# Kernel optimization log

Hardware: AMD Instinct MI355X
Metric: run time of the kernel (lower is better)

Reference implementation:

```python
import jax, jax.numpy as jnp
import numpy as np
import math

B, S, D, H = 4, 2048, 1024, 16

def setup_inputs() -> dict:
    key = jax.random.key(0)
    ks = jax.random.split(key, 8)
    scale = 1.0 / math.sqrt(D)
    return {
        "queries": jax.random.normal(ks[0], (B, S, D), dtype=jnp.float32),
        "keys": jax.random.normal(ks[1], (B, S, D), dtype=jnp.float32),
        "values": jax.random.normal(ks[2], (B, S, D), dtype=jnp.float32),
        "valid_len": jax.random.randint(ks[3], (B,), 1, S + 1, dtype=jnp.int32),
        "Wq": jax.random.normal(ks[4], (D, D), dtype=jnp.float32) * scale,
        "Wk": jax.random.normal(ks[5], (D, D), dtype=jnp.float32) * scale,
        "Wv": jax.random.normal(ks[6], (D, D), dtype=jnp.float32) * scale,
        "Wo": jax.random.normal(ks[7], (D, D), dtype=jnp.float32) * scale,
    }

def reference(queries, keys, values, valid_len, Wq, Wk, Wv, Wo):
    b, sq, _ = queries.shape
    sk = keys.shape[1]
    hd = D // H
    # projections + split heads -> [B, H, S, hd]
    q = (queries @ Wq).reshape(b, sq, H, hd).transpose(0, 2, 1, 3)
    k = (keys @ Wk).reshape(b, sk, H, hd).transpose(0, 2, 1, 3)
    v = (values @ Wv).reshape(b, sk, H, hd).transpose(0, 2, 1, 3)
    scores = jnp.einsum('bhqd,bhkd->bhqk', q, k) / math.sqrt(hd)
    # Source's sequence_mask uses query-dim length as maxlen: masks whole
    # query rows where q_pos >= valid_len (value -100000), then softmax over keys.
    row_ok = (jnp.arange(sq)[None, :] < valid_len[:, None])  # [B, Sq]
    scores = jnp.where(row_ok[:, None, :, None], scores, -100000.0)
    weights = jax.nn.softmax(scores, axis=-1)  # dropout=0.0 (eval)
    out = jnp.einsum('bhqk,bhkd->bhqd', weights, v)
    out = out.transpose(0, 2, 1, 3).reshape(b, sq, H * hd)
    return out @ Wo
```

## Files before the change

kernel.cpp:

```cpp
#include <hip/hip_runtime.h>
#include <hip/hip_bf16.h>

#define NB 4
#define NS 2048
#define ND 1024
#define NH 16
#define HDIM 64
#define NM (NB * NS)
#define MN_FULL ((size_t)NM * ND)

typedef short short8 __attribute__((ext_vector_type(8)));
typedef float f32x4 __attribute__((ext_vector_type(4)));
typedef float f32x16 __attribute__((ext_vector_type(16)));
typedef unsigned uint4v __attribute__((ext_vector_type(4)));

__device__ __forceinline__ short bf16rne(float f) {
    unsigned u = __builtin_bit_cast(unsigned, f);
    u += 0x7fff + ((u >> 16) & 1);
    return (short)(u >> 16);
}
__device__ __forceinline__ float bf2f(short s) {
    unsigned u = ((unsigned)(unsigned short)s) << 16;
    return __builtin_bit_cast(float, u);
}
__device__ __forceinline__ void gl_lds16(const short* g, short* l) {
    __builtin_amdgcn_global_load_lds(
        (const __attribute__((address_space(1))) void*)g,
        (__attribute__((address_space(3))) void*)l, 16, 0, 0);
}
__device__ __forceinline__ float fexp2(float x) {
#if __has_builtin(__builtin_amdgcn_exp2f)
    return __builtin_amdgcn_exp2f(x);
#else
    return exp2f(x);
#endif
}
__device__ __forceinline__ unsigned cvtpk(float a, float b) {
    unsigned d;
    asm("v_cvt_pk_bf16_f32 %0, %1, %2" : "=v"(d) : "v"(a), "v"(b));
    return d;
}
__device__ __forceinline__ void plswap(unsigned& x, unsigned& y) {
    asm("v_permlane32_swap_b32 %0, %1" : "+v"(x), "+v"(y));
}
__device__ __forceinline__ short8 mk8(unsigned a, unsigned b, unsigned c, unsigned d) {
    uint4v u = {a, b, c, d};
    return __builtin_bit_cast(short8, u);
}

__global__ __launch_bounds__(256)
void convA3(const float* __restrict__ A0, const float* __restrict__ A1,
            const float* __restrict__ A2, short* __restrict__ D0,
            short* __restrict__ D1, short* __restrict__ D2)
{
    const int z = blockIdx.z;
    const float* A = (z == 0) ? A0 : (z == 1) ? A1 : A2;
    short* D = (z == 0) ? D0 : (z == 1) ? D1 : D2;

    const size_t idx = (size_t)blockIdx.x * 256 + threadIdx.x;
    const int m = (int)(idx >> 7);
    const int k = (int)((idx & 127) << 3);
    const float* src = A + ((size_t)m << 10) + k;
    float4 x0 = *(const float4*)src;
    float4 x1 = *(const float4*)(src + 4);
    float xv[8] = {x0.x, x0.y, x0.z, x0.w, x1.x, x1.y, x1.z, x1.w};
    short8 hv;
#pragma unroll
    for (int j = 0; j < 8; ++j) hv[j] = bf16rne(xv[j]);
    const int ksw = (k & ~63) | ((k & 63) ^ ((m & 7) << 3));
    *(short8*)(D + ((size_t)m << 10) + ksw) = hv;
}

__global__ __launch_bounds__(256)
void convW4(const float* __restrict__ W0, const float* __restrict__ W1,
            const float* __restrict__ W2, const float* __restrict__ W3,
            short* __restrict__ Wb)
{
    const int z = blockIdx.z;
    const float* W = (z == 0) ? W0 : (z == 1) ? W1 : (z == 2) ? W2 : W3;
    short* Wh = Wb + (size_t)z * ND * ND;

    const int idx = blockIdx.x * 256 + threadIdx.x;
    const int n = idx & 1023;
    const int k = (idx >> 10) << 3;
    short8 hv;
#pragma unroll
    for (int j = 0; j < 8; ++j) hv[j] = bf16rne(W[(size_t)(k + j) * ND + n]);
    const int ksw = (k & ~63) | ((k & 63) ^ ((n & 7) << 3));
    *(short8*)(Wh + ((size_t)n << 10) + ksw) = hv;
}

template <int EPI>
__global__ __launch_bounds__(256, 3)
void gemm1(const short* __restrict__ Ah, const short* __restrict__ Bh,
           short* __restrict__ D1, float* __restrict__ Cf, float scale)
{
    __shared__ short lds[16384];
    short* AhS = lds;
    short* BhS = lds + 8192;

    const int t = threadIdx.x, w = t >> 6, l = t & 63;
    const int g = l >> 4, li = l & 15;
    const int wr = w >> 1, wc = w & 1;
    const size_t bm = (size_t)blockIdx.x * 128, bn = (size_t)blockIdx.y * 128;

    f32x4 acc[4][4];
#pragma unroll
    for (int i = 0; i < 4; ++i)
#pragma unroll
        for (int j = 0; j < 4; ++j) acc[i][j] = (f32x4){0.f, 0.f, 0.f, 0.f};

    const int srow = w * 32 + (l >> 3);
    const int schk = (l & 7) << 3;
    const short* pAh = Ah + (bm + srow) * 1024 + schk;
    const short* pBh = Bh + (bn + srow) * 1024 + schk;
    const int lbase = w * 32 * 64;

    for (int kt = 0; kt < 16; ++kt) {
        const int k0 = kt * 64;
        __syncthreads();
#pragma unroll
        for (int r = 0; r < 4; ++r) {
            const int go = r * 8 * 1024 + k0;
            const int lo_ = lbase + r * 512;
            gl_lds16(pAh + go, AhS + lo_);
            gl_lds16(pBh + go, BhS + lo_);
        }
        __syncthreads();
#pragma unroll
        for (int ks = 0; ks < 2; ++ks) {
            short8 fah[4], fbh[4];
#pragma unroll
            for (int i = 0; i < 4; ++i) {
                const int m = wr * 64 + i * 16 + li;
                const int c = (ks * 32 + g * 8) ^ ((m & 7) << 3);
                fah[i] = *(const short8*)&AhS[m * 64 + c];
                const int n = wc * 64 + i * 16 + li;
                const int cn = (ks * 32 + g * 8) ^ ((n & 7) << 3);
                fbh[i] = *(const short8*)&BhS[n * 64 + cn];
            }
#pragma unroll
            for (int i = 0; i < 4; ++i)
#pragma unroll
                for (int j = 0; j < 4; ++j)
                    acc[i][j] = __builtin_amdgcn_mfma_f32_16x16x32_bf16(fah[i], fbh[j], acc[i][j], 0, 0, 0);
        }
    }

    __syncthreads();
    float* Ofs = (float*)lds + w * 2048;
#pragma unroll
    for (int half = 0; half < 2; ++half) {
#pragma unroll
        for (int i = 0; i < 4; ++i)
#pragma unroll
            for (int jj = 0; jj < 2; ++jj)
#pragma unroll
                for (int r = 0; r < 4; ++r)
                    Ofs[(i * 16 + g * 4 + r) * 32 + jj * 16 + li] = acc[i][half * 2 + jj][r];
        if (EPI == 3) {
#pragma unroll
            for (int rr = 0; rr < 2; ++rr) {
                const int row = rr * 32 + (l >> 1);
                const int coff = (l & 1) * 16;
                const float* src = &Ofs[row * 32 + coff];
                short8 h0, h1;
#pragma unroll
                for (int jj = 0; jj < 8; ++jj) {
                    h0[jj] = bf16rne(src[jj] * scale);
                    h1[jj] = bf16rne(src[8 + jj] * scale);
                }
                const size_t rg = bm + wr * 64 + row;
                const size_t cg = bn + wc * 64 + half * 32 + coff;
                *(short8*)(D1 + rg * 1024 + cg)     = h0;
                *(short8*)(D1 + rg * 1024 + cg + 8) = h1;
            }
        } else if (EPI == 0) {
#pragma unroll
            for (int rr = 0; rr < 2; ++rr) {
                const int row = rr * 32 + (l >> 1);
                const int coff = (l & 1) * 16;
                const float* src = &Ofs[row * 32 + coff];
                const size_t rg = bm + wr * 64 + row;
                const size_t cg = bn + wc * 64 + half * 32 + coff;
#pragma unroll
                for (int q = 0; q < 4; ++q)
                    *(float4*)(Cf + rg * 1024 + cg + q * 4) = *(const float4*)(src + q * 4);
            }
        } else {
#pragma unroll
            for (int p = 0; p < 4; ++p) {
                const int nl = p * 16 + (l >> 2);
                const int mc = (l & 3) * 8;
                const float* src = &Ofs[nl * 32 + mc];
                short8 v;
#pragma unroll
                for (int jj = 0; jj < 8; ++jj) v[jj] = bf16rne(src[jj]);
                const int ng = (int)bm + wr * 64 + nl;
                const size_t mg = bn + wc * 64 + half * 32 + mc;
                const int h_ = ng >> 6, d_ = ng & 63;
                const int b_ = (int)(mg >> 11), s_ = (int)(mg & 2047);
                *(short8*)(D1 + (((size_t)(b_ * NH + h_) * HDIM + d_) << 11) + s_) = v;
            }
        }
    }
}

__global__ __launch_bounds__(256, 4)
void attn_mfma11(const short* __restrict__ Qh_g, const short* __restrict__ Kh_g,
                 const short* __restrict__ VT_g, const int* __restrict__ vlen_p,
                 short* __restrict__ AOh)
{
    __shared__ short smem[16384];
    short* Kb = smem;
    short* Vb = smem + 8192;

    const int t = threadIdx.x, w = t >> 6, l = t & 63;
    const int lh = l >> 5, lq = l & 31;

    const int lin = blockIdx.x;
    const int pair = (lin & 7) * 8 + (lin >> 7);
    const int qt = (lin >> 3) & 15;
    const int hd = pair & 15, b = pair >> 4;
    const int q0 = qt * 128;
    const int vlen = vlen_p[b];

    const short* Vbh = VT_g + (size_t)((b * NH + hd) * HDIM) * NS;

    if (q0 >= vlen) {
        float* fs = (float*)smem;
        const int d = t & 63, pc = t >> 6;
        const short* vrow = Vbh + (size_t)d * NS + pc * 512;
        float s = 0.f;
#pragma unroll 8
        for (int c = 0; c < 64; ++c) {
            short8 v = *(const short8*)(vrow + c * 8);
            float ps = 0.f;
#pragma unroll
            for (int j = 0; j < 8; ++j) ps += bf2f(v[j]);
            s += ps;
        }
        fs[pc * 64 + d] = s;
        __syncthreads();
        float* mv = fs + 256;
        if (t < 64)
            mv[t] = (fs[t] + fs[64 + t] + fs[128 + t] + fs[192 + t]) * (1.0f / 2048.0f);
        __syncthreads();

        const int row = t >> 1, hf = t & 1;
        const size_t base = ((size_t)b * NS + q0 + row) * ND + hd * HDIM;
        const int swz = (row & 7) << 3;
#pragma unroll
        for (int ch = 0; ch < 4; ++ch) {
            const int c0 = hf * 32 + ch * 8;
            short8 hv;
#pragma unroll
            for (int j = 0; j < 8; ++j) hv[j] = bf16rne(mv[c0 + j]);
            *(short8*)(AOh + base + (c0 ^ swz)) = hv;
        }
        return;
    }

    short8 qf[4];
    {
        const int qrow = q0 + w * 32 + lq;
        const size_t base = ((size_t)(b * NS) + qrow) * ND + hd * HDIM;
#pragma unroll
        for (int d = 0; d < 4; ++d)
            qf[d] = *(const short8*)(Qh_g + base + d * 16 + 8 * lh);
        if (qrow >= vlen) {
#pragma unroll
            for (int d = 0; d < 4; ++d)
#pragma unroll
                for (int j = 0; j < 8; ++j) qf[d][j] = 0;
        }
    }

    const int lrow = l >> 3, lcol = (l & 7) * 8;
    const int csw = lcol ^ (lrow << 3);
    const short* Ksrc = Kh_g + ((size_t)(b * NS) + w * 16 + lrow) * ND + hd * HDIM + csw;
    short* Kd = Kb + w * 16 * 64;

    const int vrow = w * 16 + lrow;
    const short* VsrcR = Vbh + (size_t)vrow * NS + lcol;
    const int vdst = vrow * 64 + (lcol ^ ((lrow & 7) << 3));

    float lsum = 0.f;
    f32x16 o0, o1;
#pragma unroll
    for (int i = 0; i < 16; ++i) { o0[i] = 0.f; o1[i] = 0.f; }

    gl_lds16(Ksrc, Kd);
    gl_lds16(Ksrc + 8 * ND, Kd + 512);
    {
        short8 a = *(const short8*)(VsrcR);
        short8 c = *(const short8*)(VsrcR + 8 * NS);
        *(short8*)&Vb[vdst] = a;
        *(short8*)&Vb[vdst + 512] = c;
    }

    const int r7s = (lq & 7) << 3;

    for (int kt = 0; kt < NS / 64; ++kt) {
        const int cur = kt & 1;
        __syncthreads();

        short8 vn0, vn1;
        const bool pf = (kt < NS / 64 - 1);
        if (pf) {
            const short* s_ = Ksrc + (size_t)(kt + 1) * 64 * ND;
            short* d_ = Kd + (cur ^ 1) * 4096;
            gl_lds16(s_, d_);
            gl_lds16(s_ + 8 * ND, d_ + 512);
            vn0 = *(const short8*)(VsrcR + (kt + 1) * 64);
            vn1 = *(const short8*)(VsrcR + (kt + 1) * 64 + 8 * NS);
        }

#pragma unroll
        for (int kb = 0; kb < 2; ++kb) {
            const int rbase = cur * 4096 + (kb * 32 + lq) * 64;
            short8 kf0 = *(const short8*)&Kb[rbase + ((0  + 8 * lh) ^ r7s)];
            short8 kf1 = *(const short8*)&Kb[rbase + ((16 + 8 * lh) ^ r7s)];
            short8 kf2 = *(const short8*)&Kb[rbase + ((32 + 8 * lh) ^ r7s)];
            short8 kf3 = *(const short8*)&Kb[rbase + ((48 + 8 * lh) ^ r7s)];

            const int vb0 = cur * 4096 + lq * 64;
            const int vb1 = cur * 4096 + (32 + lq) * 64;
            short8 v00 = *(const short8*)&Vb[vb0 + ((kb * 32 + 8 * lh) ^ r7s)];
            short8 v01 = *(const short8*)&Vb[vb0 + ((kb * 32 + 16 + 8 * lh) ^ r7s)];
            short8 v10 = *(const short8*)&Vb[vb1 + ((kb * 32 + 8 * lh) ^ r7s)];
            short8 v11 = *(const short8*)&Vb[vb1 + ((kb * 32 + 16 + 8 * lh) ^ r7s)];

            f32x16 acc;
#pragma unroll
            for (int i = 0; i < 16; ++i) acc[i] = 0.f;
            acc = __builtin_amdgcn_mfma_f32_32x32x16_bf16(kf0, qf[0], acc, 0, 0, 0);
            acc = __builtin_amdgcn_mfma_f32_32x32x16_bf16(kf1, qf[1], acc, 0, 0, 0);
            acc = __builtin_amdgcn_mfma_f32_32x32x16_bf16(kf2, qf[2], acc, 0, 0, 0);
            acc = __builtin_amdgcn_mfma_f32_32x32x16_bf16(kf3, qf[3], acc, 0, 0, 0);

            float e[16];
#pragma unroll
            for (int i = 0; i < 16; ++i) e[i] = fexp2(acc[i]);
            float s4 = 0.f;
#pragma unroll
            for (int i = 0; i < 16; ++i) s4 += e[i];
            lsum += s4;

            unsigned d0 = cvtpk(e[0],  e[1]);
            unsigned d1 = cvtpk(e[2],  e[3]);
            unsigned d2 = cvtpk(e[4],  e[5]);
            unsigned d3 = cvtpk(e[6],  e[7]);
            unsigned d4 = cvtpk(e[8],  e[9]);
            unsigned d5 = cvtpk(e[10], e[11]);
            unsigned d6 = cvtpk(e[12], e[13]);
            unsigned d7 = cvtpk(e[14], e[15]);
            plswap(d0, d2);
            plswap(d1, d3);
            plswap(d4, d6);
            plswap(d5, d7);
            short8 B0 = mk8(d0, d1, d2, d3);
            short8 B1 = mk8(d4, d5, d6, d7);

            o0 = __builtin_amdgcn_mfma_f32_32x32x16_bf16(v00, B0, o0, 0, 0, 0);
            o0 = __builtin_amdgcn_mfma_f32_32x32x16_bf16(v01, B1, o0, 0, 0, 0);
            o1 = __builtin_amdgcn_mfma_f32_32x32x16_bf16(v10, B0, o1, 0, 0, 0);
            o1 = __builtin_amdgcn_mfma_f32_32x32x16_bf16(v11, B1, o1, 0, 0, 0);
        }

        if (pf) {
            *(short8*)&Vb[(cur ^ 1) * 4096 + vdst]       = vn0;
            *(short8*)&Vb[(cur ^ 1) * 4096 + vdst + 512] = vn1;
        }
    }

    const float lt = lsum + __shfl_xor(lsum, 32);
    const float rin = 1.0f / lt;

    __syncthreads();
    float* Ob = (float*)smem + w * 1152;
    const int qe = l >> 1, dp = l & 1;
    const size_t aorow = (size_t)b * NS + q0 + w * 32 + qe;
    const int r7e = (qe & 7) << 3;
#pragma unroll
    for (int dt = 0; dt < 2; ++dt) {
        const f32x16 ov = dt ? o1 : o0;
#pragma unroll
        for (int r = 0; r < 16; ++r)
            Ob[lq * 36 + (r & 3) + 8 * (r >> 2) + 4 * lh] = ov[r] * rin;
        float xv[16];
#pragma unroll
        for (int c = 0; c < 4; ++c) {
            float4 x = *(const float4*)&Ob[qe * 36 + dp * 16 + c * 4];
            xv[c * 4 + 0] = x.x; xv[c * 4 + 1] = x.y;
            xv[c * 4 + 2] = x.z; xv[c * 4 + 3] = x.w;
        }
        short8 hv0, hv1;
#pragma unroll
        for (int j = 0; j < 8; ++j) {
            hv0[j] = bf16rne(xv[j]);
            hv1[j] = bf16rne(xv[8 + j]);
        }
        const size_t base = aorow * ND + hd * HDIM;
        *(short8*)(AOh + base + ((dt * 32 + dp * 16 + 0) ^ r7e)) = hv0;
        *(short8*)(AOh + base + ((dt * 32 + dp * 16 + 8) ^ r7e)) = hv1;
    }
}

extern "C" void kernel_launch(void* const* d_in, const int* in_sizes, int n_in,
                              void* d_out, int out_size, void* d_ws, size_t ws_size,
                              hipStream_t stream)
{
    const float* queries = (const float*)d_in[0];
    const float* keys    = (const float*)d_in[1];
    const float* values  = (const float*)d_in[2];
    const int*   vlen    = (const int*)d_in[3];
    const float* Wq      = (const float*)d_in[4];
    const float* Wk      = (const float*)d_in[5];
    const float* Wv      = (const float*)d_in[6];
    const float* Wo      = (const float*)d_in[7];
    float* out           = (float*)d_out;

    short* A0  = (short*)d_ws;
    short* A1  = A0 + MN_FULL;
    short* A2  = A1 + MN_FULL;
    short* W4  = A2 + MN_FULL;
    short* Qhi = W4 + 4 * (size_t)ND * ND;
    short* Khi = Qhi + MN_FULL;
    short* VT  = Khi + MN_FULL;
    short* AOh = A0;

    const int gA = (int)(MN_FULL / 8 / 256);
    const int gW = (int)((size_t)ND * ND / 8 / 256);
    dim3 gP(NM / 128, ND / 128);
    dim3 gV(ND / 128, NM / 128);

    const float QSCALE = 0.125f * 1.44269504089f;

    convA3<<<dim3(gA, 1, 3), 256, 0, stream>>>(queries, keys, values, A0, A1, A2);
    convW4<<<dim3(gW, 1, 4), 256, 0, stream>>>(Wq, Wk, Wv, Wo, W4);

    gemm1<3><<<gP, 256, 0, stream>>>(A0, W4,                         Qhi, nullptr, QSCALE);
    gemm1<3><<<gP, 256, 0, stream>>>(A1, W4 + (size_t)ND * ND,       Khi, nullptr, 1.0f);
    gemm1<2><<<gV, 256, 0, stream>>>(W4 + 2 * (size_t)ND * ND, A2,   VT,  nullptr, 1.0f);

    attn_mfma11<<<dim3(1024), 256, 0, stream>>>(Qhi, Khi, VT, vlen, AOh);

    gemm1<0><<<gP, 256, 0, stream>>>(AOh, W4 + 3 * (size_t)ND * ND, nullptr, out, 1.0f);
}
```

Baseline: 194.8 us.

## Fuse fp32-to-bf16 input conversion into projection GEMM tile loads

Removes the separate activation conversion kernel and has the projection GEMMs read fp32 queries/keys/values directly, converting to bf16 with packed cvt instructions before storing swizzled tiles into LDS. This eliminates a full write and re-read of three bf16 activation buffers. In exchange the GEMM reads twice the bytes per reuse of the fp32 operand and replaces async global-to-LDS loads with synchronous register round-trips, which may expose load latency.

```diff
diff --git a/kernel.cpp b/kernel.cpp
--- a/kernel.cpp
+++ b/kernel.cpp
@@ -47,28 +47,12 @@
     uint4v u = {a, b, c, d};
     return __builtin_bit_cast(short8, u);
 }
-
-__global__ __launch_bounds__(256)
-void convA3(const float* __restrict__ A0, const float* __restrict__ A1,
-            const float* __restrict__ A2, short* __restrict__ D0,
-            short* __restrict__ D1, short* __restrict__ D2)
-{
-    const int z = blockIdx.z;
-    const float* A = (z == 0) ? A0 : (z == 1) ? A1 : A2;
-    short* D = (z == 0) ? D0 : (z == 1) ? D1 : D2;
-
-    const size_t idx = (size_t)blockIdx.x * 256 + threadIdx.x;
-    const int m = (int)(idx >> 7);
-    const int k = (int)((idx & 127) << 3);
-    const float* src = A + ((size_t)m << 10) + k;
-    float4 x0 = *(const float4*)src;
-    float4 x1 = *(const float4*)(src + 4);
-    float xv[8] = {x0.x, x0.y, x0.z, x0.w, x1.x, x1.y, x1.z, x1.w};
-    short8 hv;
-#pragma unroll
-    for (int j = 0; j < 8; ++j) hv[j] = bf16rne(xv[j]);
-    const int ksw = (k & ~63) | ((k & 63) ^ ((m & 7) << 3));
-    *(short8*)(D + ((size_t)m << 10) + ksw) = hv;
+__device__ __forceinline__ short8 cvt8(const float* s) {
+    float4 x0 = *(const float4*)s;
+    float4 x1 = *(const float4*)(s + 4);
+    uint4v u = {cvtpk(x0.x, x0.y), cvtpk(x0.z, x0.w),
+                cvtpk(x1.x, x1.y), cvtpk(x1.z, x1.w)};
+    return __builtin_bit_cast(short8, u);
 }
 
 __global__ __launch_bounds__(256)
@@ -90,9 +74,9 @@
     *(short8*)(Wh + ((size_t)n << 10) + ksw) = hv;
 }
 
-template <int EPI>
+template <int EPI, bool AF32, bool BF32>
 __global__ __launch_bounds__(256, 3)
-void gemm1(const short* __restrict__ Ah, const short* __restrict__ Bh,
+void gemm2(const void* __restrict__ Ap, const void* __restrict__ Bp,
            short* __restrict__ D1, float* __restrict__ Cf, float scale)
 {
     __shared__ short lds[16384];
@@ -112,9 +96,15 @@
 
     const int srow = w * 32 + (l >> 3);
     const int schk = (l & 7) << 3;
-    const short* pAh = Ah + (bm + srow) * 1024 + schk;
-    const short* pBh = Bh + (bn + srow) * 1024 + schk;
     const int lbase = w * 32 * 64;
+    const int xdst = lbase + (l >> 3) * 64 + (schk ^ (((l >> 3) & 7) << 3));
+
+    const short* pAh = nullptr; const float* pAf = nullptr;
+    const short* pBh = nullptr; const float* pBf = nullptr;
+    if constexpr (AF32) pAf = (const float*)Ap + (bm + srow) * 1024 + schk;
+    else                pAh = (const short*)Ap + (bm + srow) * 1024 + schk;
+    if constexpr (BF32) pBf = (const float*)Bp + (bn + srow) * 1024 + schk;
+    else                pBh = (const short*)Bp + (bn + srow) * 1024 + schk;
 
     for (int kt = 0; kt < 16; ++kt) {
         const int k0 = kt * 64;
@@ -122,9 +112,10 @@
 #pragma unroll
         for (int r = 0; r < 4; ++r) {
             const int go = r * 8 * 1024 + k0;
-            const int lo_ = lbase + r * 512;
-            gl_lds16(pAh + go, AhS + lo_);
-            gl_lds16(pBh + go, BhS + lo_);
+            if constexpr (AF32) *(short8*)&AhS[xdst + r * 512] = cvt8(pAf + go);
+            else                gl_lds16(pAh + go, AhS + lbase + r * 512);
+            if constexpr (BF32) *(short8*)&BhS[xdst + r * 512] = cvt8(pBf + go);
+            else                gl_lds16(pBh + go, BhS + lbase + r * 512);
         }
         __syncthreads();
 #pragma unroll
@@ -421,30 +412,25 @@
     const float* Wo      = (const float*)d_in[7];
     float* out           = (float*)d_out;
 
-    short* A0  = (short*)d_ws;
-    short* A1  = A0 + MN_FULL;
-    short* A2  = A1 + MN_FULL;
-    short* W4  = A2 + MN_FULL;
+    short* W4  = (short*)d_ws;
     short* Qhi = W4 + 4 * (size_t)ND * ND;
     short* Khi = Qhi + MN_FULL;
     short* VT  = Khi + MN_FULL;
-    short* AOh = A0;
-
-    const int gA = (int)(MN_FULL / 8 / 256);
+    short* AOh = VT + MN_FULL;
+
     const int gW = (int)((size_t)ND * ND / 8 / 256);
     dim3 gP(NM / 128, ND / 128);
     dim3 gV(ND / 128, NM / 128);
 
     const float QSCALE = 0.125f * 1.44269504089f;
 
-    convA3<<<dim3(gA, 1, 3), 256, 0, stream>>>(queries, keys, values, A0, A1, A2);
     convW4<<<dim3(gW, 1, 4), 256, 0, stream>>>(Wq, Wk, Wv, Wo, W4);
 
-    gemm1<3><<<gP, 256, 0, stream>>>(A0, W4,                         Qhi, nullptr, QSCALE);
-    gemm1<3><<<gP, 256, 0, stream>>>(A1, W4 + (size_t)ND * ND,       Khi, nullptr, 1.0f);
-    gemm1<2><<<gV, 256, 0, stream>>>(W4 + 2 * (size_t)ND * ND, A2,   VT,  nullptr, 1.0f);
+    gemm2<3, true, false><<<gP, 256, 0, stream>>>(queries, W4, Qhi, nullptr, QSCALE);
+    gemm2<3, true, false><<<gP, 256, 0, stream>>>(keys, W4 + (size_t)ND * ND, Khi, nullptr, 1.0f);
+    gemm2<2, false, true><<<gV, 256, 0, stream>>>(W4 + 2 * (size_t)ND * ND, values, VT, nullptr, 1.0f);
 
     attn_mfma11<<<dim3(1024), 256, 0, stream>>>(Qhi, Khi, VT, vlen, AOh);
 
-    gemm1<0><<<gP, 256, 0, stream>>>(AOh, W4 + 3 * (size_t)ND * ND, nullptr, out, 1.0f);
-}
+    gemm2<0, false, false><<<gP, 256, 0, stream>>>(AOh, W4 + 3 * (size_t)ND * ND, nullptr, out, 1.0f);
+}
```

After: 202.3 us. 1.04x slower.
